# Optimization experiments

Hardware: AMD Instinct MI355X
Metric: run time of the kernel (lower is better)

The kernel has to match this reference:

```python
import jax, jax.numpy as jnp
import numpy as np

TOL = 1e-4
EPS = 1e-8


def sinkhorn(cost):
    # cost: (T, L) float32. Matches torch loop: d0 over rows, d1 over cols.
    cost = jnp.exp(cost)
    T, L = cost.shape
    d0 = jnp.ones((T,), jnp.float32)
    d1 = jnp.ones((L,), jnp.float32)

    def cond(state):
        _, _, err = state
        return err > TOL

    def body(state):
        d0, d1, _ = state
        d0n = (1.0 / T) / (cost @ d1 + EPS)          # sum(d1*cost, axis=1)
        d1n = (1.0 / L) / (d0n @ cost + EPS)         # sum(d0[:,None]*cost, axis=0)
        err = jnp.mean(jnp.abs(d1 - d1n))
        return (d0n, d1n, err)

    d0, d1, _ = jax.lax.while_loop(cond, body, (d0, d1, jnp.float32(1e9)))
    return d1[None, :] * cost * d0[:, None]


def setup_inputs() -> dict:
    key = jax.random.key(0)
    k1, k2 = jax.random.split(key)
    T, H, E, L = 8192, 2048, 8, 16
    x = jax.random.normal(k1, (T, H), dtype=jnp.float32)
    w1 = jax.random.normal(k2, (E, H, L), dtype=jnp.float32) * 0.02
    tokens_per_expert = jnp.full((E,), T // E, dtype=jnp.int32)  # sums to T
    return {"x": x, "w1": w1, "tokens_per_expert": tokens_per_expert, "top_k": 2}


def reference(x, w1, tokens_per_expert, top_k):
    T = x.shape[0]
    E = w1.shape[0]
    # grouped GEMM: token t uses weight slab of its expert (tokens are
    # contiguous per expert, counts given by tokens_per_expert)
    eid = jnp.repeat(jnp.arange(E), tokens_per_expert, total_repeat_length=T)  # (T,)
    logits_all = jnp.einsum('th,ehl->tel', x, w1)                 # (T, E, L)
    logits = jnp.take_along_axis(logits_all, eid[:, None, None], axis=1)[:, 0, :]  # (T, L)

    # training path: Sinkhorn (no-grad in torch) selects indices, softmax gives scores
    norm_logits = sinkhorn(logits.astype(jnp.float32))
    _, indices = jax.lax.top_k(norm_logits, top_k)                # (T, k)
    if top_k == 1:
        act = jax.nn.sigmoid(logits)
    else:
        act = jax.nn.softmax(logits.astype(jnp.float32), axis=-1).astype(logits.dtype)
    scores = jnp.take_along_axis(act, indices, axis=1)            # (T, k)
    return scores, indices
```

## Files before the change

### kernel.cpp

```cpp
#include <hip/hip_runtime.h>
#include <hip/hip_cooperative_groups.h>

namespace cg = cooperative_groups;

constexpr int T_TOK = 8192;
constexpr int H_DIM = 2048;
constexpr int E_NUM = 8;
constexpr int L_DIM = 16;
constexpr int NBLK2 = 32;

constexpr int NSB    = 8;
constexpr int HSLICE = 64;

constexpr size_t WS_COST = 0;
constexpr size_t WS_D0   = (size_t)T_TOK * L_DIM;
constexpr size_t WS_D1   = WS_D0 + T_TOK;
constexpr size_t WS_PART = WS_D1 + L_DIM;
constexpr size_t WS_PB   = WS_PART + 2 * NBLK2 * 16;

__global__ __launch_bounds__(256) void k1a(const float* __restrict__ x,
                                           const float* __restrict__ w1,
                                           const int* __restrict__ tpe,
                                           float* __restrict__ pb) {
    const int tid  = threadIdx.x;
    const int wv   = tid >> 6;
    const int lane = tid & 63;
    const int sb   = blockIdx.x & (NSB - 1);
    const int tset = blockIdx.x >> 3;
    const int t    = tset * 64 + lane;
    const int h0   = sb * 256 + wv * HSLICE;

    __shared__ float smem[4352];

    int e = 0;
    {
        int accum = 0;
        #pragma unroll
        for (int i = 0; i < E_NUM - 1; ++i) {
            accum += tpe[i];
            e += (t >= accum) ? 1 : 0;
        }
    }
    const int e0 = __builtin_amdgcn_readfirstlane(e);

    {
        const float4* wsrc =
            reinterpret_cast<const float4*>(w1 + ((size_t)e0 * H_DIM + sb * 256) * L_DIM);
        #pragma unroll
        for (int i = 0; i < 4; ++i) {
            const int idx = i * 256 + tid;
            *reinterpret_cast<float4*>(&smem[idx * 4]) = wsrc[idx];
        }
    }

    const float4* __restrict__ xp =
        reinterpret_cast<const float4*>(x + (size_t)t * H_DIM + h0);
    float4 xs[16];
    #pragma unroll
    for (int i = 0; i < 16; ++i) xs[i] = xp[i];

    __syncthreads();

    float acc[16];
    #pragma unroll
    for (int l = 0; l < 16; ++l) acc[l] = 0.f;

    const float* wl = &smem[(size_t)wv * HSLICE * 16];
    #pragma unroll
    for (int i = 0; i < 16; ++i) {
        const float xv[4] = {xs[i].x, xs[i].y, xs[i].z, xs[i].w};
        #pragma unroll
        for (int j = 0; j < 4; ++j) {
            const int h = i * 4 + j;
            const float4* wrow = reinterpret_cast<const float4*>(wl + h * 16);
            #pragma unroll
            for (int q = 0; q < 4; ++q) {
                const float4 wv4 = wrow[q];
                acc[q * 4 + 0] += xv[j] * wv4.x;
                acc[q * 4 + 1] += xv[j] * wv4.y;
                acc[q * 4 + 2] += xv[j] * wv4.z;
                acc[q * 4 + 3] += xv[j] * wv4.w;
            }
        }
    }

    __syncthreads();
    #pragma unroll
    for (int l = 0; l < 16; ++l)
        smem[((size_t)wv * 64 + lane) * 17 + l] = acc[l];
    __syncthreads();

    #pragma unroll
    for (int i = 0; i < 4; ++i) {
        const int p   = tid + i * 256;
        const int tok = p >> 4;
        const int l   = p & 15;
        const float s = smem[(0 * 64 + tok) * 17 + l] + smem[(1 * 64 + tok) * 17 + l]
                      + smem[(2 * 64 + tok) * 17 + l] + smem[(3 * 64 + tok) * 17 + l];
        pb[(size_t)sb * (T_TOK * L_DIM) + (size_t)tset * 1024 + p] = s;
    }
}

__global__ __launch_bounds__(256) void k_sinkhorn(float* __restrict__ ws) {
    cg::grid_group grid = cg::this_grid();

    float* costw = ws + WS_COST;
    float* d0ws  = ws + WS_D0;
    float* d1ws  = ws + WS_D1;
    float* part  = ws + WS_PART;
    const float* pb = ws + WS_PB;

    const int t    = blockIdx.x * blockDim.x + threadIdx.x;
    const int wv   = threadIdx.x >> 6;
    const int lane = threadIdx.x & 63;

    float c[16];
    {
        float4 a0 = {0, 0, 0, 0}, a1 = {0, 0, 0, 0}, a2 = {0, 0, 0, 0}, a3 = {0, 0, 0, 0};
        #pragma unroll
        for (int b = 0; b < NSB; ++b) {
            const float4* pr =
                reinterpret_cast<const float4*>(pb + (size_t)b * (T_TOK * L_DIM) + (size_t)t * 16);
            const float4 p0 = pr[0], p1 = pr[1], p2 = pr[2], p3 = pr[3];
            a0.x += p0.x; a0.y += p0.y; a0.z += p0.z; a0.w += p0.w;
            a1.x += p1.x; a1.y += p1.y; a1.z += p1.z; a1.w += p1.w;
            a2.x += p2.x; a2.y += p2.y; a2.z += p2.z; a2.w += p2.w;
            a3.x += p3.x; a3.y += p3.y; a3.z += p3.z; a3.w += p3.w;
        }
        const float sv[16] = {a0.x, a0.y, a0.z, a0.w, a1.x, a1.y, a1.z, a1.w,
                              a2.x, a2.y, a2.z, a2.w, a3.x, a3.y, a3.z, a3.w};
        #pragma unroll
        for (int l = 0; l < 16; ++l) c[l] = expf(sv[l]);
        float4* cw = reinterpret_cast<float4*>(costw + (size_t)t * 16);
        cw[0] = make_float4(c[0], c[1], c[2], c[3]);
        cw[1] = make_float4(c[4], c[5], c[6], c[7]);
        cw[2] = make_float4(c[8], c[9], c[10], c[11]);
        cw[3] = make_float4(c[12], c[13], c[14], c[15]);
    }

    float d1[16];
    #pragma unroll
    for (int l = 0; l < 16; ++l) d1[l] = 1.f;

    __shared__ float s_part[4][16];
    __shared__ float s_d1n[16];

    float d0n = 0.f;
    float err = 1e9f;
    int it = 0;

    do {
        float s = 0.f;
        #pragma unroll
        for (int l = 0; l < 16; ++l) s += c[l] * d1[l];
        d0n = (1.f / (float)T_TOK) / (s + 1e-8f);

        float con[16];
        #pragma unroll
        for (int l = 0; l < 16; ++l) con[l] = d0n * c[l];
        #pragma unroll
        for (int m = 1; m < 64; m <<= 1) {
            #pragma unroll
            for (int l = 0; l < 16; ++l) con[l] += __shfl_xor(con[l], m, 64);
        }
        if (lane == 0) {
            #pragma unroll
            for (int l = 0; l < 16; ++l) s_part[wv][l] = con[l];
        }
        __syncthreads();

        const int p = it & 1;
        if (threadIdx.x < 16) {
            const float bs = s_part[0][threadIdx.x] + s_part[1][threadIdx.x]
                           + s_part[2][threadIdx.x] + s_part[3][threadIdx.x];
            part[(size_t)p * (NBLK2 * 16) + (size_t)blockIdx.x * 16 + threadIdx.x] = bs;
        }

        grid.sync();

        if (threadIdx.x < 16) {
            float tot = 0.f;
            #pragma unroll 4
            for (int b = 0; b < NBLK2; ++b)
                tot += part[(size_t)p * (NBLK2 * 16) + (size_t)b * 16 + threadIdx.x];
            s_d1n[threadIdx.x] = (1.f / (float)L_DIM) / (tot + 1e-8f);
        }
        __syncthreads();

        float esum = 0.f;
        #pragma unroll
        for (int l = 0; l < 16; ++l) {
            const float nv = s_d1n[l];
            esum += fabsf(d1[l] - nv);
            d1[l] = nv;
        }
        err = esum * (1.f / 16.f);
        ++it;
    } while (err > 1e-4f && it < 512);

    d0ws[t] = d0n;
    if (blockIdx.x == 0 && threadIdx.x < 16) d1ws[threadIdx.x] = s_d1n[threadIdx.x];
}

__global__ __launch_bounds__(256) void k_final(const float* __restrict__ ws,
                                               float* __restrict__ out) {
    const float* cost = ws + WS_COST;
    const float* d0ws = ws + WS_D0;
    const float* d1ws = ws + WS_D1;

    const int t = blockIdx.x * blockDim.x + threadIdx.x;

    float c[16];
    {
        const float4* cr = reinterpret_cast<const float4*>(cost + (size_t)t * 16);
        const float4 c0 = cr[0], c1 = cr[1], c2 = cr[2], c3 = cr[3];
        c[0]=c0.x; c[1]=c0.y; c[2]=c0.z; c[3]=c0.w;
        c[4]=c1.x; c[5]=c1.y; c[6]=c1.z; c[7]=c1.w;
        c[8]=c2.x; c[9]=c2.y; c[10]=c2.z; c[11]=c2.w;
        c[12]=c3.x; c[13]=c3.y; c[14]=c3.z; c[15]=c3.w;
    }
    const float d0v = d0ws[t];

    float v1 = -__builtin_inff(), v2 = -__builtin_inff();
    float a1 = 0.f, a2 = 0.f;
    int   i1 = 0, i2 = 0;
    float ssum = 0.f;
    #pragma unroll
    for (int l = 0; l < 16; ++l) {
        ssum += c[l];
        const float nv = (d1ws[l] * c[l]) * d0v;
        if (nv > v1) { v2 = v1; i2 = i1; a2 = a1; v1 = nv; i1 = l; a1 = c[l]; }
        else if (nv > v2) { v2 = nv; i2 = l; a2 = c[l]; }
    }
    const float sc1 = a1 / ssum;
    const float sc2 = a2 / ssum;

    out[(size_t)t * 2 + 0] = sc1;
    out[(size_t)t * 2 + 1] = sc2;
    out[(size_t)2 * T_TOK + (size_t)t * 2 + 0] = (float)i1;
    out[(size_t)2 * T_TOK + (size_t)t * 2 + 1] = (float)i2;
}

extern "C" void kernel_launch(void* const* d_in, const int* in_sizes, int n_in,
                              void* d_out, int out_size, void* d_ws, size_t ws_size,
                              hipStream_t stream) {
    const float* x   = (const float*)d_in[0];
    const float* w1  = (const float*)d_in[1];
    const int*   tpe = (const int*)d_in[2];
    float* ws  = (float*)d_ws;
    float* out = (float*)d_out;

    k1a<<<dim3(128 * NSB), dim3(256), 0, stream>>>(x, w1, tpe, ws + WS_PB);

    {
        void* args[] = { (void*)&ws };
        hipLaunchCooperativeKernel((void*)k_sinkhorn, dim3(NBLK2), dim3(256),
                                   args, 0, stream);
    }

    k_final<<<dim3(T_TOK / 256), dim3(256), 0, stream>>>(ws, out);
}
```

Baseline: 75.40 us.

## Restructure GEMM tiling, replace grid.sync with tagged atomic slab, fuse final kernel

```diff
diff --git a/kernel.cpp b/kernel.cpp
--- a/kernel.cpp
+++ b/kernel.cpp
@@ -1,98 +1,118 @@
 #include <hip/hip_runtime.h>
-#include <hip/hip_cooperative_groups.h>
-
-namespace cg = cooperative_groups;
 
 constexpr int T_TOK = 8192;
 constexpr int H_DIM = 2048;
 constexpr int E_NUM = 8;
 constexpr int L_DIM = 16;
-constexpr int NBLK2 = 32;
-
-constexpr int NSB    = 8;
-constexpr int HSLICE = 64;
-
-constexpr size_t WS_COST = 0;
-constexpr size_t WS_D0   = (size_t)T_TOK * L_DIM;
-constexpr size_t WS_D1   = WS_D0 + T_TOK;
-constexpr size_t WS_PART = WS_D1 + L_DIM;
-constexpr size_t WS_PB   = WS_PART + 2 * NBLK2 * 16;
-
-__global__ __launch_bounds__(256) void k1a(const float* __restrict__ x,
-                                           const float* __restrict__ w1,
-                                           const int* __restrict__ tpe,
-                                           float* __restrict__ pb) {
+
+constexpr int NSB   = 8;
+constexpr int NBLK2 = 8;
+constexpr int BLK2  = 1024;
+
+constexpr size_t WS_SLAB = 0;
+constexpr size_t WS_PB   = 512;
+
+__global__ __launch_bounds__(256, 4) void k1a(const float* __restrict__ x,
+                                              const float* __restrict__ w1,
+                                              const int* __restrict__ tpe,
+                                              float* __restrict__ pb) {
     const int tid  = threadIdx.x;
-    const int wv   = tid >> 6;
+    const int sb   = blockIdx.x & 7;
+    const int tset = blockIdx.x >> 3;
+    const int wvi  = tid >> 6;
     const int lane = tid & 63;
-    const int sb   = blockIdx.x & (NSB - 1);
-    const int tset = blockIdx.x >> 3;
-    const int t    = tset * 64 + lane;
-    const int h0   = sb * 256 + wv * HSLICE;
+    const int quad = lane >> 2;
+    const int a    = lane & 3;
+    const int h0   = sb * 256;
 
     __shared__ float smem[4352];
 
     int e = 0;
     {
+        const int tok0 = tset * 64;
         int accum = 0;
         #pragma unroll
         for (int i = 0; i < E_NUM - 1; ++i) {
             accum += tpe[i];
-            e += (t >= accum) ? 1 : 0;
+            e += (tok0 >= accum) ? 1 : 0;
         }
     }
     const int e0 = __builtin_amdgcn_readfirstlane(e);
 
     {
         const float4* wsrc =
-            reinterpret_cast<const float4*>(w1 + ((size_t)e0 * H_DIM + sb * 256) * L_DIM);
-        #pragma unroll
-        for (int i = 0; i < 4; ++i) {
-            const int idx = i * 256 + tid;
-            *reinterpret_cast<float4*>(&smem[idx * 4]) = wsrc[idx];
-        }
-    }
-
-    const float4* __restrict__ xp =
-        reinterpret_cast<const float4*>(x + (size_t)t * H_DIM + h0);
-    float4 xs[16];
-    #pragma unroll
-    for (int i = 0; i < 16; ++i) xs[i] = xp[i];
+            reinterpret_cast<const float4*>(w1 + ((size_t)e0 * H_DIM + h0) * L_DIM);
+        #pragma unroll
+        for (int itr = 0; itr < 4; ++itr) {
+            const int idx = itr * 256 + tid;
+            const float4 v = wsrc[idx];
+            const int h  = idx >> 2;
+            const int l0 = (idx & 3) * 4;
+            smem[(l0 + 0) * 260 + h] = v.x;
+            smem[(l0 + 1) * 260 + h] = v.y;
+            smem[(l0 + 2) * 260 + h] = v.z;
+            smem[(l0 + 3) * 260 + h] = v.w;
+        }
+    }
+
+    const float4* __restrict__ x4 = reinterpret_cast<const float4*>(x);
+    const size_t xbase = (size_t)(tset * 64 + quad) * (H_DIM / 4) + (size_t)(h0 + wvi * 64) / 4;
+
+    float acc[4][16];
+    #pragma unroll
+    for (int r = 0; r < 4; ++r)
+        #pragma unroll
+        for (int l = 0; l < 16; ++l) acc[r][l] = 0.f;
+
+    float4 xk[4], xn[4];
+    #pragma unroll
+    for (int r = 0; r < 4; ++r)
+        xk[r] = x4[xbase + (size_t)r * 16 * (H_DIM / 4) + a];
 
     __syncthreads();
 
-    float acc[16];
-    #pragma unroll
-    for (int l = 0; l < 16; ++l) acc[l] = 0.f;
-
-    const float* wl = &smem[(size_t)wv * HSLICE * 16];
-    #pragma unroll
-    for (int i = 0; i < 16; ++i) {
-        const float xv[4] = {xs[i].x, xs[i].y, xs[i].z, xs[i].w};
-        #pragma unroll
-        for (int j = 0; j < 4; ++j) {
-            const int h = i * 4 + j;
-            const float4* wrow = reinterpret_cast<const float4*>(wl + h * 16);
-            #pragma unroll
-            for (int q = 0; q < 4; ++q) {
-                const float4 wv4 = wrow[q];
-                acc[q * 4 + 0] += xv[j] * wv4.x;
-                acc[q * 4 + 1] += xv[j] * wv4.y;
-                acc[q * 4 + 2] += xv[j] * wv4.z;
-                acc[q * 4 + 3] += xv[j] * wv4.w;
-            }
-        }
+    #pragma unroll
+    for (int k = 0; k < 4; ++k) {
+        if (k < 3) {
+            #pragma unroll
+            for (int r = 0; r < 4; ++r)
+                xn[r] = x4[xbase + (size_t)r * 16 * (H_DIM / 4) + a + 4 * (k + 1)];
+        }
+        const int c4 = wvi * 64 + (a + 4 * k) * 4;
+        #pragma unroll
+        for (int l = 0; l < 16; ++l) {
+            const float4 w4 = *reinterpret_cast<const float4*>(&smem[l * 260 + c4]);
+            #pragma unroll
+            for (int r = 0; r < 4; ++r)
+                acc[r][l] += xk[r].x * w4.x + xk[r].y * w4.y
+                           + xk[r].z * w4.z + xk[r].w * w4.w;
+        }
+        #pragma unroll
+        for (int r = 0; r < 4; ++r) xk[r] = xn[r];
+    }
+
+    #pragma unroll
+    for (int m = 1; m <= 2; m <<= 1) {
+        #pragma unroll
+        for (int r = 0; r < 4; ++r)
+            #pragma unroll
+            for (int l = 0; l < 16; ++l)
+                acc[r][l] += __shfl_xor(acc[r][l], m, 64);
     }
 
     __syncthreads();
     #pragma unroll
-    for (int l = 0; l < 16; ++l)
-        smem[((size_t)wv * 64 + lane) * 17 + l] = acc[l];
+    for (int r = 0; r < 4; ++r) {
+        const int tok = r * 16 + quad;
+        #pragma unroll
+        for (int j = 0; j < 4; ++j)
+            smem[(wvi * 64 + tok) * 17 + a * 4 + j] = acc[r][a * 4 + j];
+    }
     __syncthreads();
 
     #pragma unroll
     for (int i = 0; i < 4; ++i) {
-        const int p   = tid + i * 256;
+        const int p   = i * 256 + tid;
         const int tok = p >> 4;
         const int l   = p & 15;
         const float s = smem[(0 * 64 + tok) * 17 + l] + smem[(1 * 64 + tok) * 17 + l]
@@ -101,22 +121,19 @@
     }
 }
 
-__global__ __launch_bounds__(256) void k_sinkhorn(float* __restrict__ ws) {
-    cg::grid_group grid = cg::this_grid();
-
-    float* costw = ws + WS_COST;
-    float* d0ws  = ws + WS_D0;
-    float* d1ws  = ws + WS_D1;
-    float* part  = ws + WS_PART;
+__global__ __launch_bounds__(1024) void k_sinkhorn(float* __restrict__ ws,
+                                                   float* __restrict__ out) {
+    unsigned long long* slab = reinterpret_cast<unsigned long long*>(ws + WS_SLAB);
     const float* pb = ws + WS_PB;
 
-    const int t    = blockIdx.x * blockDim.x + threadIdx.x;
-    const int wv   = threadIdx.x >> 6;
-    const int lane = threadIdx.x & 63;
+    const int tid  = threadIdx.x;
+    const int t    = blockIdx.x * BLK2 + tid;
+    const int wv   = tid >> 6;
+    const int lane = tid & 63;
 
     float c[16];
     {
-        float4 a0 = {0, 0, 0, 0}, a1 = {0, 0, 0, 0}, a2 = {0, 0, 0, 0}, a3 = {0, 0, 0, 0};
+        float4 a0 = {0,0,0,0}, a1 = {0,0,0,0}, a2 = {0,0,0,0}, a3 = {0,0,0,0};
         #pragma unroll
         for (int b = 0; b < NSB; ++b) {
             const float4* pr =
@@ -131,18 +148,14 @@
                               a2.x, a2.y, a2.z, a2.w, a3.x, a3.y, a3.z, a3.w};
         #pragma unroll
         for (int l = 0; l < 16; ++l) c[l] = expf(sv[l]);
-        float4* cw = reinterpret_cast<float4*>(costw + (size_t)t * 16);
-        cw[0] = make_float4(c[0], c[1], c[2], c[3]);
-        cw[1] = make_float4(c[4], c[5], c[6], c[7]);
-        cw[2] = make_float4(c[8], c[9], c[10], c[11]);
-        cw[3] = make_float4(c[12], c[13], c[14], c[15]);
     }
 
     float d1[16];
     #pragma unroll
     for (int l = 0; l < 16; ++l) d1[l] = 1.f;
 
-    __shared__ float s_part[4][16];
+    __shared__ float s_wpart[16][16];
+    __shared__ float s_bpart[NBLK2][16];
     __shared__ float s_d1n[16];
 
     float d0n = 0.f;
@@ -165,25 +178,37 @@
         }
         if (lane == 0) {
             #pragma unroll
-            for (int l = 0; l < 16; ++l) s_part[wv][l] = con[l];
+            for (int l = 0; l < 16; ++l) s_wpart[wv][l] = con[l];
         }
         __syncthreads();
 
         const int p = it & 1;
-        if (threadIdx.x < 16) {
-            const float bs = s_part[0][threadIdx.x] + s_part[1][threadIdx.x]
-                           + s_part[2][threadIdx.x] + s_part[3][threadIdx.x];
-            part[(size_t)p * (NBLK2 * 16) + (size_t)blockIdx.x * 16 + threadIdx.x] = bs;
-        }
-
-        grid.sync();
-
-        if (threadIdx.x < 16) {
+        if (tid < 16) {
+            float bs = 0.f;
+            #pragma unroll
+            for (int w = 0; w < 16; ++w) bs += s_wpart[w][tid];
+            const unsigned long long v =
+                ((unsigned long long)(unsigned)it << 32) |
+                (unsigned long long)__float_as_uint(bs);
+            __hip_atomic_store(&slab[(size_t)p * (NBLK2 * 16) + (size_t)blockIdx.x * 16 + tid],
+                               v, __ATOMIC_RELAXED, __HIP_MEMORY_SCOPE_AGENT);
+        }
+        if (tid < NBLK2 * 16) {
+            unsigned long long v;
+            int spins = 0;
+            do {
+                v = __hip_atomic_load(&slab[(size_t)p * (NBLK2 * 16) + tid],
+                                      __ATOMIC_RELAXED, __HIP_MEMORY_SCOPE_AGENT);
+            } while ((unsigned)(v >> 32) != (unsigned)it && ++spins < (1 << 22));
+            s_bpart[tid >> 4][tid & 15] = __uint_as_float((unsigned)(v & 0xffffffffull));
+        }
+        __syncthreads();
+
+        if (tid < 16) {
             float tot = 0.f;
-            #pragma unroll 4
-            for (int b = 0; b < NBLK2; ++b)
-                tot += part[(size_t)p * (NBLK2 * 16) + (size_t)b * 16 + threadIdx.x];
-            s_d1n[threadIdx.x] = (1.f / (float)L_DIM) / (tot + 1e-8f);
+            #pragma unroll
+            for (int b = 0; b < NBLK2; ++b) tot += s_bpart[b][tid];
+            s_d1n[tid] = (1.f / (float)L_DIM) / (tot + 1e-8f);
         }
         __syncthreads();
 
@@ -198,29 +223,6 @@
         ++it;
     } while (err > 1e-4f && it < 512);
 
-    d0ws[t] = d0n;
-    if (blockIdx.x == 0 && threadIdx.x < 16) d1ws[threadIdx.x] = s_d1n[threadIdx.x];
-}
-
-__global__ __launch_bounds__(256) void k_final(const float* __restrict__ ws,
-                                               float* __restrict__ out) {
-    const float* cost = ws + WS_COST;
-    const float* d0ws = ws + WS_D0;
-    const float* d1ws = ws + WS_D1;
-
-    const int t = blockIdx.x * blockDim.x + threadIdx.x;
-
-    float c[16];
-    {
-        const float4* cr = reinterpret_cast<const float4*>(cost + (size_t)t * 16);
-        const float4 c0 = cr[0], c1 = cr[1], c2 = cr[2], c3 = cr[3];
-        c[0]=c0.x; c[1]=c0.y; c[2]=c0.z; c[3]=c0.w;
-        c[4]=c1.x; c[5]=c1.y; c[6]=c1.z; c[7]=c1.w;
-        c[8]=c2.x; c[9]=c2.y; c[10]=c2.z; c[11]=c2.w;
-        c[12]=c3.x; c[13]=c3.y; c[14]=c3.z; c[15]=c3.w;
-    }
-    const float d0v = d0ws[t];
-
     float v1 = -__builtin_inff(), v2 = -__builtin_inff();
     float a1 = 0.f, a2 = 0.f;
     int   i1 = 0, i2 = 0;
@@ -228,15 +230,12 @@
     #pragma unroll
     for (int l = 0; l < 16; ++l) {
         ssum += c[l];
-        const float nv = (d1ws[l] * c[l]) * d0v;
+        const float nv = (d1[l] * c[l]) * d0n;
         if (nv > v1) { v2 = v1; i2 = i1; a2 = a1; v1 = nv; i1 = l; a1 = c[l]; }
         else if (nv > v2) { v2 = nv; i2 = l; a2 = c[l]; }
     }
-    const float sc1 = a1 / ssum;
-    const float sc2 = a2 / ssum;
-
-    out[(size_t)t * 2 + 0] = sc1;
-    out[(size_t)t * 2 + 1] = sc2;
+    out[(size_t)t * 2 + 0] = a1 / ssum;
+    out[(size_t)t * 2 + 1] = a2 / ssum;
     out[(size_t)2 * T_TOK + (size_t)t * 2 + 0] = (float)i1;
     out[(size_t)2 * T_TOK + (size_t)t * 2 + 1] = (float)i2;
 }
@@ -253,10 +252,8 @@
     k1a<<<dim3(128 * NSB), dim3(256), 0, stream>>>(x, w1, tpe, ws + WS_PB);
 
     {
-        void* args[] = { (void*)&ws };
-        hipLaunchCooperativeKernel((void*)k_sinkhorn, dim3(NBLK2), dim3(256),
+        void* args[] = { (void*)&ws, (void*)&out };
+        hipLaunchCooperativeKernel((void*)k_sinkhorn, dim3(NBLK2), dim3(BLK2),
                                    args, 0, stream);
     }
-
-    k_final<<<dim3(T_TOK / 256), dim3(256), 0, stream>>>(ws, out);
 }
```

Measured after the change: 178.9 us. 137% more time.
